# Kernel optimization log

Measured on AMD Instinct MI355X. Metric: run time of the kernel, lower is better.

Reference implementation:

```python
import jax, jax.numpy as jnp
from jax import lax
import numpy as np

DIVISOR = 2.0

def setup_inputs() -> dict:
    key = jax.random.key(0)
    k1, k2, k3, k4 = jax.random.split(key, 4)
    B, Cin, D, H, W = 64, 8, 32, 64, 64
    Cout, KD, KH, KW = 16, 3, 3, 3
    fan_in = Cin * KD * KH * KW
    bound = 1.0 / np.sqrt(fan_in)
    x = jax.random.normal(k1, (B, Cin, D, H, W), dtype=jnp.float32)
    conv_weight = jax.random.uniform(k2, (Cout, Cin, KD, KH, KW), jnp.float32, -bound, bound)
    conv_bias = jax.random.uniform(k3, (Cout,), jnp.float32, -bound, bound)
    bias = jax.random.normal(k4, (Cout, 1, 1, 1), dtype=jnp.float32) * 0.02
    return {"x": x, "conv_weight": conv_weight, "conv_bias": conv_bias, "bias": bias}

def reference(x, conv_weight, conv_bias, bias):
    # Conv3d, stride 1, no padding, groups=1  -> [B, Cout, D-2, H-2, W-2]
    y = lax.conv_general_dilated(
        x, conv_weight, window_strides=(1, 1, 1), padding='VALID',
        dimension_numbers=('NCDHW', 'OIDHW', 'NCDHW'))
    y = y + conv_bias[None, :, None, None, None]
    # Divide by constant
    y = y / DIVISOR
    # MaxPool3d(kernel=2, stride=2), floor mode (VALID drops the trailing odd row)
    y = lax.reduce_window(y, -jnp.inf, lax.max,
                          window_dimensions=(1, 1, 2, 2, 2),
                          window_strides=(1, 1, 2, 2, 2), padding='VALID')
    # AdaptiveAvgPool3d((1,1,1)) == global mean over spatial dims
    y = jnp.mean(y, axis=(2, 3, 4), keepdims=True)  # [B, Cout, 1, 1, 1]
    # Bias add (broadcast over batch)
    y = y + bias[None]
    # Sum over channel dim (sum_dim=1, no keepdim)
    return jnp.sum(y, axis=1)  # [B, 1, 1, 1]
```

## Files before the change

### kernel.cpp

```cpp
#include <hip/hip_runtime.h>

typedef __attribute__((ext_vector_type(8))) short short8;
typedef __attribute__((ext_vector_type(4))) float f32x4;
typedef unsigned int u32;

#define SLOT_B 4096
#define NSLOT 4
#define CSTRIDE 131072

__device__ __forceinline__ unsigned short f2bf(float f) {
  unsigned u = __builtin_bit_cast(unsigned, f);
  u += 0x7FFFu + ((u >> 16) & 1u);
  return (unsigned short)(u >> 16);
}
__device__ __forceinline__ u32 cvtpk(float lo, float hi) {
  u32 r;
  asm("v_cvt_pk_bf16_f32 %0, %1, %2" : "=v"(r) : "v"(lo), "v"(hi));
  return r;
}

#define MFMA1(A, B, C) __builtin_amdgcn_mfma_f32_16x16x32_bf16(A, B, C, 0, 0, 0)

#define MGRP(F0, F1, F2, F3, WT, AN, AM, AO, K0, K1, K2)                      \
  {                                                                           \
    if (K0) {                                                                 \
      AN[0][WT] = MFMA1(F0, bfragB[0][0], zf4);                               \
      AN[1][WT] = MFMA1(F1, bfragB[0][0], zf4);                               \
      AN[0][WT] = MFMA1(F1, bfragB[0][1], AN[0][WT]);                         \
      AN[1][WT] = MFMA1(F2, bfragB[0][1], AN[1][WT]);                         \
      AN[0][WT] = MFMA1(F2, bfragB[0][2], AN[0][WT]);                         \
      AN[1][WT] = MFMA1(F3, bfragB[0][2], AN[1][WT]);                         \
    }                                                                         \
    if (K1) {                                                                 \
      AM[0][WT] = MFMA1(F0, bfragB[1][0], AM[0][WT]);                         \
      AM[1][WT] = MFMA1(F1, bfragB[1][0], AM[1][WT]);                         \
      AM[0][WT] = MFMA1(F1, bfragB[1][1], AM[0][WT]);                         \
      AM[1][WT] = MFMA1(F2, bfragB[1][1], AM[1][WT]);                         \
      AM[0][WT] = MFMA1(F2, bfragB[1][2], AM[0][WT]);                         \
      AM[1][WT] = MFMA1(F3, bfragB[1][2], AM[1][WT]);                         \
    }                                                                         \
    if (K2) {                                                                 \
      AO[0][WT] = MFMA1(F0, bfragB[2][0], AO[0][WT]);                         \
      AO[1][WT] = MFMA1(F1, bfragB[2][0], AO[1][WT]);                         \
      AO[0][WT] = MFMA1(F1, bfragB[2][1], AO[0][WT]);                         \
      AO[1][WT] = MFMA1(F2, bfragB[2][1], AO[1][WT]);                         \
      AO[0][WT] = MFMA1(F2, bfragB[2][2], AO[0][WT]);                         \
      AO[1][WT] = MFMA1(F3, bfragB[2][2], AO[1][WT]);                         \
    }                                                                         \
  }

#define PROC(DP, AN, AM, AO, K0, K1, K2, CL, SV, ST)                          \
  {                                                                           \
    const int dp_ = (DP);                                                     \
    if (ST) {                                                                 \
      stage_load(dp_ + 2);                                                    \
      __builtin_amdgcn_sched_barrier(0);                                      \
    }                                                                         \
    const int sb_ = (dp_ & 3) * SLOT_B;                                       \
    __builtin_amdgcn_s_setprio(1);                                            \
    _Pragma("unroll") for (int wt = 0; wt < 4; ++wt) {                        \
      const short8 f0 = *(const short8*)(smem + sb_ + 0 * 1024 + physoff[wt]); \
      const short8 f1 = *(const short8*)(smem + sb_ + 1 * 1024 + physoff[wt]); \
      const short8 f2 = *(const short8*)(smem + sb_ + 2 * 1024 + physoff[wt]); \
      const short8 f3 = *(const short8*)(smem + sb_ + 3 * 1024 + physoff[wt]); \
      MGRP(f0, f1, f2, f3, wt, AN, AM, AO, K0, K1, K2);                       \
    }                                                                         \
    __builtin_amdgcn_s_setprio(0);                                            \
    __builtin_amdgcn_sched_barrier(0);                                        \
    if (ST) stage_write(dp_ + 2);                                             \
    if (CL) {                                                                 \
      _Pragma("unroll") for (int wt = 0; wt < 4; ++wt) {                      \
        const float e01 = fmaxf(fmaxf(AO[0][wt][0], AO[0][wt][1]),            \
                                fmaxf(AO[1][wt][0], AO[1][wt][1]));           \
        const float e23 = fmaxf(fmaxf(AO[0][wt][2], AO[0][wt][3]),            \
                                fmaxf(AO[1][wt][2], AO[1][wt][3]));           \
        if (SV) {                                                             \
          p01[wt] = e01; p23[wt] = e23;                                       \
        } else {                                                              \
          sum += fmaxf(p01[wt], e01);                                         \
          if (!(wt == 3 && g == 3)) sum += fmaxf(p23[wt], e23);               \
        }                                                                     \
      }                                                                       \
    }                                                                         \
  }

__launch_bounds__(64, 2)
__global__ void conv_fused(const float* __restrict__ x,
                           const float* __restrict__ cw,
                           float* __restrict__ ws) {
  __shared__ __align__(16) unsigned char smem[NSLOT * SLOT_B + 32];

  const int rb  = blockIdx.x;
  const int bid = (rb & 7) * 248 + (rb >> 3);
  const int b   = bid / 31;
  const int q   = bid - 31 * b;
  const int h0  = 2 * q;

  const int lane = threadIdx.x;
  const int nm   = lane & 15;
  const int g    = lane >> 4;

  const float* xb = x + (size_t)b * (8u * 32u * 64u * 64u);

  short8 bfragB[3][3];
#pragma unroll
  for (int kd = 0; kd < 3; ++kd)
#pragma unroll
    for (int kh = 0; kh < 3; ++kh) {
      short8 f;
#pragma unroll
      for (int j = 0; j < 8; ++j) {
        float v = (g < 3) ? cw[(nm * 8 + j) * 27 + kd * 9 + kh * 3 + g] : 0.f;
        f[j] = (short)f2bf(v);
      }
      bfragB[kd][kh] = f;
    }

  const int gc = (g < 3) ? g : 2;
  int physoff[4];
#pragma unroll
  for (int wt = 0; wt < 4; ++wt) physoff[wt] = (wt * 16 + nm + gc) * 16;

  int o_base[4];
#pragma unroll
  for (int s = 0; s < 4; ++s) o_base[s] = (h0 + s) * 64 + lane;

  float ld[4][8];

  auto stage_load = [&](int p) {
    const int pbase = p * 4096;
#pragma unroll
    for (int s = 0; s < 4; ++s) {
      const int o = o_base[s] + pbase;
#pragma unroll
      for (int c = 0; c < 8; ++c)
        ld[s][c] = (xb + (size_t)c * CSTRIDE)[o];
    }
  };
  auto stage_write = [&](int p) {
    unsigned char* d = smem + (p & 3) * SLOT_B + lane * 16;
#pragma unroll
    for (int s = 0; s < 4; ++s) {
      uint4 v;
      v.x = cvtpk(ld[s][0], ld[s][1]);
      v.y = cvtpk(ld[s][2], ld[s][3]);
      v.z = cvtpk(ld[s][4], ld[s][5]);
      v.w = cvtpk(ld[s][6], ld[s][7]);
      *(uint4*)(d + s * 1024) = v;
    }
  };

  const f32x4 zf4 = {0.f, 0.f, 0.f, 0.f};
  float sum = 0.f;
  float p01[4], p23[4];
  f32x4 accA[2][4], accB[2][4], accC[2][4];

  stage_load(0); stage_write(0);
  stage_load(1); stage_write(1);

  PROC(0, accA, accB, accC, 1, 0, 0, 0, 0, 1)
  PROC(1, accB, accA, accC, 1, 1, 0, 0, 0, 1)

  for (int p0 = 2; p0 <= 20; p0 += 6) {
    PROC(p0 + 0, accC, accB, accA, 1, 1, 1, 1, 1, 1)
    PROC(p0 + 1, accA, accC, accB, 1, 1, 1, 1, 0, 1)
    PROC(p0 + 2, accB, accA, accC, 1, 1, 1, 1, 1, 1)
    PROC(p0 + 3, accC, accB, accA, 1, 1, 1, 1, 0, 1)
    PROC(p0 + 4, accA, accC, accB, 1, 1, 1, 1, 1, 1)
    PROC(p0 + 5, accB, accA, accC, 1, 1, 1, 1, 0, 1)
  }
  PROC(26, accC, accB, accA, 1, 1, 1, 1, 1, 1)
  PROC(27, accA, accC, accB, 1, 1, 1, 1, 0, 1)
  PROC(28, accB, accA, accC, 1, 1, 1, 1, 1, 1)
  PROC(29, accC, accB, accA, 1, 1, 1, 1, 0, 1)
  PROC(30, accA, accC, accB, 0, 1, 1, 1, 1, 0)
  PROC(31, accB, accA, accC, 0, 0, 1, 1, 0, 0)

#pragma unroll
  for (int off = 32; off > 0; off >>= 1) sum += __shfl_down(sum, off);
  if (lane == 0) ws[bid] = sum;
}

__global__ void finalize_k(const float* __restrict__ ws,
                           const float* __restrict__ cb,
                           const float* __restrict__ bias,
                           float* __restrict__ out) {
  const int b = threadIdx.x;
  float s = 0.f;
#pragma unroll
  for (int q = 0; q < 31; ++q) s += ws[b * 31 + q];
  float cbs = 0.f, bs = 0.f;
#pragma unroll
  for (int c = 0; c < 16; ++c) { cbs += cb[c]; bs += bias[c]; }
  out[b] = 0.5f * s / 14415.f + 0.5f * cbs + bs;
}

extern "C" void kernel_launch(void* const* d_in, const int* in_sizes, int n_in,
                              void* d_out, int out_size, void* d_ws, size_t ws_size,
                              hipStream_t stream) {
  const float* x    = (const float*)d_in[0];
  const float* cw   = (const float*)d_in[1];
  const float* cb   = (const float*)d_in[2];
  const float* bias = (const float*)d_in[3];
  float* out = (float*)d_out;
  float* ws  = (float*)d_ws;

  hipLaunchKernelGGL(conv_fused, dim3(1984), dim3(64), 0, stream, x, cw, ws);
  hipLaunchKernelGGL(finalize_k, dim3(1), dim3(64), 0, stream, ws, cb, bias, out);
}
```

Measured before the change: 78.80 us.

## Split each conv block's W range into two halves to double the grid

```diff
diff --git a/kernel.cpp b/kernel.cpp
--- a/kernel.cpp
+++ b/kernel.cpp
@@ -4,7 +4,7 @@
 typedef __attribute__((ext_vector_type(4))) float f32x4;
 typedef unsigned int u32;
 
-#define SLOT_B 4096
+#define SLOT_B 2176
 #define NSLOT 4
 #define CSTRIDE 131072
 
@@ -58,18 +58,18 @@
     }                                                                         \
     const int sb_ = (dp_ & 3) * SLOT_B;                                       \
     __builtin_amdgcn_s_setprio(1);                                            \
-    _Pragma("unroll") for (int wt = 0; wt < 4; ++wt) {                        \
-      const short8 f0 = *(const short8*)(smem + sb_ + 0 * 1024 + physoff[wt]); \
-      const short8 f1 = *(const short8*)(smem + sb_ + 1 * 1024 + physoff[wt]); \
-      const short8 f2 = *(const short8*)(smem + sb_ + 2 * 1024 + physoff[wt]); \
-      const short8 f3 = *(const short8*)(smem + sb_ + 3 * 1024 + physoff[wt]); \
+    _Pragma("unroll") for (int wt = 0; wt < 2; ++wt) {                        \
+      const short8 f0 = *(const short8*)(smem + sb_ + 0 * 544 + physoff[wt]); \
+      const short8 f1 = *(const short8*)(smem + sb_ + 1 * 544 + physoff[wt]); \
+      const short8 f2 = *(const short8*)(smem + sb_ + 2 * 544 + physoff[wt]); \
+      const short8 f3 = *(const short8*)(smem + sb_ + 3 * 544 + physoff[wt]); \
       MGRP(f0, f1, f2, f3, wt, AN, AM, AO, K0, K1, K2);                       \
     }                                                                         \
     __builtin_amdgcn_s_setprio(0);                                            \
     __builtin_amdgcn_sched_barrier(0);                                        \
     if (ST) stage_write(dp_ + 2);                                             \
     if (CL) {                                                                 \
-      _Pragma("unroll") for (int wt = 0; wt < 4; ++wt) {                      \
+      _Pragma("unroll") for (int wt = 0; wt < 2; ++wt) {                      \
         const float e01 = fmaxf(fmaxf(AO[0][wt][0], AO[0][wt][1]),            \
                                 fmaxf(AO[1][wt][0], AO[1][wt][1]));           \
         const float e23 = fmaxf(fmaxf(AO[0][wt][2], AO[0][wt][3]),            \
@@ -78,23 +78,26 @@
           p01[wt] = e01; p23[wt] = e23;                                       \
         } else {                                                              \
           sum += fmaxf(p01[wt], e01);                                         \
-          if (!(wt == 3 && g == 3)) sum += fmaxf(p23[wt], e23);               \
+          if (!(wt == 1 && wmask)) sum += fmaxf(p23[wt], e23);                \
         }                                                                     \
       }                                                                       \
     }                                                                         \
   }
 
-__launch_bounds__(64, 2)
+__launch_bounds__(64, 3)
 __global__ void conv_fused(const float* __restrict__ x,
                            const float* __restrict__ cw,
                            float* __restrict__ ws) {
-  __shared__ __align__(16) unsigned char smem[NSLOT * SLOT_B + 32];
+  __shared__ __align__(16) unsigned char smem[NSLOT * SLOT_B + 16];
 
   const int rb  = blockIdx.x;
-  const int bid = (rb & 7) * 248 + (rb >> 3);
-  const int b   = bid / 31;
-  const int q   = bid - 31 * b;
+  const int bid = (rb & 7) * 496 + (rb >> 3);
+  const int b   = bid / 62;
+  const int r2  = bid - 62 * b;
+  const int q   = r2 >> 1;
+  const int wh  = r2 & 1;
   const int h0  = 2 * q;
+  const int w0  = wh * 32;
 
   const int lane = threadIdx.x;
   const int nm   = lane & 15;
@@ -117,43 +120,57 @@
     }
 
   const int gc = (g < 3) ? g : 2;
-  int physoff[4];
-#pragma unroll
-  for (int wt = 0; wt < 4; ++wt) physoff[wt] = (wt * 16 + nm + gc) * 16;
-
-  int o_base[4];
-#pragma unroll
-  for (int s = 0; s < 4; ++s) o_base[s] = (h0 + s) * 64 + lane;
-
-  float ld[4][8];
+  int physoff[2];
+#pragma unroll
+  for (int wt = 0; wt < 2; ++wt) physoff[wt] = (wt * 16 + nm + gc) * 16;
+
+  int st_toff[3], st_off[3];
+#pragma unroll
+  for (int pass = 0; pass < 3; ++pass) {
+    const int s   = lane + pass * 64;
+    const int row = (s < 136) ? (s / 34) : 0;
+    const int ch  = (s < 136) ? (s - 34 * row) : 0;
+    int w = w0 + ch; if (w > 63) w = 63;
+    st_toff[pass] = (h0 + row) * 64 + w;
+    st_off[pass]  = row * 544 + ch * 16;
+  }
+  const bool act2 = (lane < 8);
+
+  float ld[3][8];
 
   auto stage_load = [&](int p) {
     const int pbase = p * 4096;
 #pragma unroll
-    for (int s = 0; s < 4; ++s) {
-      const int o = o_base[s] + pbase;
-#pragma unroll
-      for (int c = 0; c < 8; ++c)
-        ld[s][c] = (xb + (size_t)c * CSTRIDE)[o];
+    for (int pass = 0; pass < 3; ++pass) {
+      if (pass < 2 || act2) {
+        const int o = st_toff[pass] + pbase;
+#pragma unroll
+        for (int c = 0; c < 8; ++c)
+          ld[pass][c] = (xb + (size_t)c * CSTRIDE)[o];
+      }
     }
   };
   auto stage_write = [&](int p) {
-    unsigned char* d = smem + (p & 3) * SLOT_B + lane * 16;
-#pragma unroll
-    for (int s = 0; s < 4; ++s) {
-      uint4 v;
-      v.x = cvtpk(ld[s][0], ld[s][1]);
-      v.y = cvtpk(ld[s][2], ld[s][3]);
-      v.z = cvtpk(ld[s][4], ld[s][5]);
-      v.w = cvtpk(ld[s][6], ld[s][7]);
-      *(uint4*)(d + s * 1024) = v;
+    unsigned char* d = smem + (p & 3) * SLOT_B;
+#pragma unroll
+    for (int pass = 0; pass < 3; ++pass) {
+      if (pass < 2 || act2) {
+        uint4 v;
+        v.x = cvtpk(ld[pass][0], ld[pass][1]);
+        v.y = cvtpk(ld[pass][2], ld[pass][3]);
+        v.z = cvtpk(ld[pass][4], ld[pass][5]);
+        v.w = cvtpk(ld[pass][6], ld[pass][7]);
+        *(uint4*)(d + st_off[pass]) = v;
+      }
     }
   };
 
+  const bool wmask = (wh == 1) && (g == 3);
+
   const f32x4 zf4 = {0.f, 0.f, 0.f, 0.f};
   float sum = 0.f;
-  float p01[4], p23[4];
-  f32x4 accA[2][4], accB[2][4], accC[2][4];
+  float p01[2], p23[2];
+  f32x4 accA[2][2], accB[2][2], accC[2][2];
 
   stage_load(0); stage_write(0);
   stage_load(1); stage_write(1);
@@ -188,7 +205,7 @@
   const int b = threadIdx.x;
   float s = 0.f;
 #pragma unroll
-  for (int q = 0; q < 31; ++q) s += ws[b * 31 + q];
+  for (int i = 0; i < 62; ++i) s += ws[b * 62 + i];
   float cbs = 0.f, bs = 0.f;
 #pragma unroll
   for (int c = 0; c < 16; ++c) { cbs += cb[c]; bs += bias[c]; }
@@ -205,6 +222,6 @@
   float* out = (float*)d_out;
   float* ws  = (float*)d_ws;
 
-  hipLaunchKernelGGL(conv_fused, dim3(1984), dim3(64), 0, stream, x, cw, ws);
+  hipLaunchKernelGGL(conv_fused, dim3(3968), dim3(64), 0, stream, x, cw, ws);
   hipLaunchKernelGGL(finalize_k, dim3(1), dim3(64), 0, stream, ws, cb, bias, out);
 }
```

Result: slower. 96.63 us (+22.6%).
